# Kernel tuning notes

Hardware: AMD Instinct MI355X
Metric: run time of the kernel (lower is better)

## Reference

```python
import jax, jax.numpy as jnp
import numpy as np

B, R, A, S, SR = 128, 1024, 512, 196, 64


def _linear(x, w, b):
    return x @ w.T + b


def _lstm_cell(x, h, c, wih, whh, bih, bhh):
    # torch.nn.LSTMCell gate order: i, f, g, o
    g = x @ wih.T + bih + h @ whh.T + bhh
    i, f, gg, o = jnp.split(g, 4, axis=-1)
    c2 = jax.nn.sigmoid(f) * c + jax.nn.sigmoid(i) * jnp.tanh(gg)
    h2 = jax.nn.sigmoid(o) * jnp.tanh(c2)
    return h2, c2


def _attention(h, att_feats, p_att, mask, h2att_w, h2att_b, aw, ab):
    att_h = _linear(h, h2att_w, h2att_b)[:, None, :]            # [B,1,A]
    dot = jnp.tanh(p_att + att_h)                               # [B,S,A]
    e = jnp.einsum('bsa,a->bs', dot, aw[0]) + ab[0]             # alpha_net
    w = jax.nn.softmax(e, axis=1)
    w = w * mask
    w = w / jnp.sum(w, axis=1, keepdims=True)
    return jnp.einsum('bs,bsd->bd', w, att_feats)


def setup_inputs() -> dict:
    key = jax.random.key(0)
    ks = iter(jax.random.split(key, 80))
    def rn(shape, scale=1.0):
        return jax.random.normal(next(ks), shape, dtype=jnp.float32) * scale
    w = 0.02  # weight init scale
    inp = {
        'xt': rn((B, R)), 'state_h': rn((2, B, R)), 'state_c': rn((2, B, R)),
        'fc_feats': rn((B, R)),
        'att_feats': rn((B, S, R)), 'obj_feats': rn((B, S, R)),
        'attr_feats': rn((B, S, R)), 'rela_feats': rn((B, SR, R)),
        'p_obj_feats': rn((B, S, A)), 'p_attr_feats': rn((B, S, A)),
        'p_rela_feats': rn((B, SR, A)),
        'att_masks': jnp.ones((B, S), jnp.float32),
        'rela_masks': jnp.ones((B, SR), jnp.float32),
        'att_wih': rn((4*R, 3*R), w), 'att_whh': rn((4*R, R), w),
        'att_bih': rn((4*R,), w), 'att_bhh': rn((4*R,), w),
        'lang_wih': rn((4*R, 4*R), w), 'lang_whh': rn((4*R, R), w),
        'lang_bih': rn((4*R,), w), 'lang_bhh': rn((4*R,), w),
        'xt2_w': rn((R, R), w), 'xt2_b': rn((R,), w),
        'h_att2_w': rn((R, R), w), 'h_att2_b': rn((R,), w),
        'r_i2h_w': rn((R, 4*R), w), 'r_i2h_b': rn((R,), w),
        'r_h2h_w': rn((R, R), w), 'r_h2h_b': rn((R,), w),
        'huu_w': rn((R, 3*R), w), 'huu_b': rn((R,), w),
        'obj_h2att_w': rn((A, R), w), 'obj_h2att_b': rn((A,), w),
        'obj_alpha_w': rn((1, A), w), 'obj_alpha_b': rn((1,), w),
        'attr_h2att_w': rn((A, R), w), 'attr_h2att_b': rn((A,), w),
        'attr_alpha_w': rn((1, A), w), 'attr_alpha_b': rn((1,), w),
        'rela_h2att_w': rn((A, R), w), 'rela_h2att_b': rn((A,), w),
        'rela_alpha_w': rn((1, A), w), 'rela_alpha_b': rn((1,), w),
        'fr_lin_w': rn((R, R), w), 'fr_lin_b': rn((R,), w),
        'fr_emb_w': rn((R, R), w), 'fr_emb_b': rn((R,), w),
        'ho_lin_w': rn((R, R), w), 'ho_lin_b': rn((R,), w),
        'ho_emb_w': rn((R, R), w), 'ho_emb_b': rn((R,), w),
        'ada_alpha_w': rn((1, R), w), 'ada_alpha_b': rn((1,), w),
        'cfe_w': rn((R, A), w), 'cfe_b': rn((R,), w),
    }
    return inp


def reference(xt, state_h, state_c, fc_feats, att_feats, obj_feats, attr_feats,
              rela_feats, p_obj_feats, p_attr_feats, p_rela_feats, att_masks,
              rela_masks, att_wih, att_whh, att_bih, att_bhh, lang_wih,
              lang_whh, lang_bih, lang_bhh, xt2_w, xt2_b, h_att2_w, h_att2_b,
              r_i2h_w, r_i2h_b, r_h2h_w, r_h2h_b, huu_w, huu_b, obj_h2att_w,
              obj_h2att_b, obj_alpha_w, obj_alpha_b, attr_h2att_w,
              attr_h2att_b, attr_alpha_w, attr_alpha_b, rela_h2att_w,
              rela_h2att_b, rela_alpha_w, rela_alpha_b, fr_lin_w, fr_lin_b,
              fr_emb_w, fr_emb_b, ho_lin_w, ho_lin_b, ho_emb_w, ho_emb_b,
              ada_alpha_w, ada_alpha_b, cfe_w, cfe_b):
    # eval mode: all dropouts are identity
    prev_h = state_h[1]
    att_in = jnp.concatenate([prev_h, fc_feats, xt], axis=1)            # [B,3R]
    h_att_raw, c_att = _lstm_cell(att_in, state_h[0], state_c[0],
                                  att_wih, att_whh, att_bih, att_bhh)
    h_att = _linear(xt, xt2_w, xt2_b) + _linear(h_att_raw, h_att2_w, h_att2_b)
    att_obj = _attention(h_att, obj_feats, p_obj_feats, att_masks,
                         obj_h2att_w, obj_h2att_b, obj_alpha_w, obj_alpha_b)
    att_attr = _attention(h_att, attr_feats, p_attr_feats, att_masks,
                          attr_h2att_w, attr_h2att_b, attr_alpha_w, attr_alpha_b)
    att_rela = _attention(h_att, rela_feats, p_rela_feats, rela_masks,
                          rela_h2att_w, rela_h2att_b, rela_alpha_w, rela_alpha_b)
    lang_in = jnp.concatenate([h_att, att_obj, att_attr, att_rela], axis=1)  # [B,4R]
    h_lang, c_lang = _lstm_cell(lang_in, state_h[1], state_c[1],
                                lang_wih, lang_whh, lang_bih, lang_bhh)
    tanh_mt = jnp.tanh(c_lang)
    n5 = _linear(lang_in, r_i2h_w, r_i2h_b) + _linear(state_h[1], r_h2h_w, r_h2h_b)
    st = jax.nn.sigmoid(n5) * tanh_mt                                    # [B,R]
    # AdaAtt_attention(h_lang, st, att_feats, p_obj_feats)
    cfe = _linear(p_obj_feats, cfe_w, cfe_b)                             # [B,S,R]
    fake_region = jax.nn.relu(_linear(st, fr_lin_w, fr_lin_b))           # [B,R]
    fr_embed = _linear(fake_region, fr_emb_w, fr_emb_b)
    ho = jnp.tanh(_linear(h_lang, ho_lin_w, ho_lin_b))
    ho_embed = _linear(ho, ho_emb_w, ho_emb_b)
    img_all = jnp.concatenate([fake_region[:, None, :], att_feats], axis=1)    # [B,S+1,R]
    img_all_embed = jnp.concatenate([fr_embed[:, None, :], cfe], axis=1)
    hA = jnp.tanh(img_all_embed + ho_embed[:, None, :])
    e = jnp.einsum('bsr,r->bs', hA, ada_alpha_w[0]) + ada_alpha_b[0]
    PI = jax.nn.softmax(e, axis=1)                                       # [B,S+1]
    visAtt = jnp.einsum('bs,bsd->bd', PI, img_all)
    beta = PI[:, -1:]
    c_t_hat = beta * fake_region + (1.0 - beta) * visAtt
    output = _linear(jnp.concatenate([h_att, h_lang, c_t_hat], axis=1), huu_w, huu_b)
    new_h = jnp.stack([h_att, h_lang])
    new_c = jnp.stack([c_att, c_lang])
    return output, new_h, new_c
```

## Files before the change

kernel.cpp:

```cpp
#include <hip/hip_runtime.h>
#include <cstddef>

#define B 128
#define R 1024

typedef __attribute__((ext_vector_type(8))) short short8;
typedef __attribute__((ext_vector_type(4))) float f32x4;

__device__ __forceinline__ float sigf(float x) { return 1.0f / (1.0f + __expf(-x)); }

__device__ __forceinline__ short f2bf(float f) {
    unsigned int u = __float_as_uint(f);
    u += 0x7fff + ((u >> 16) & 1);
    return (short)(u >> 16);
}

__device__ __forceinline__ short8 cvt8(float4 u, float4 v) {
    short8 r;
    r[0] = f2bf(u.x); r[1] = f2bf(u.y); r[2] = f2bf(u.z); r[3] = f2bf(u.w);
    r[4] = f2bf(v.x); r[5] = f2bf(v.y); r[6] = f2bf(v.z); r[7] = f2bf(v.w);
    return r;
}

__device__ __forceinline__ void gll16(const void* g, void* l) {
    __builtin_amdgcn_global_load_lds(
        (const __attribute__((address_space(1))) unsigned int*)g,
        (__attribute__((address_space(3))) unsigned int*)l, 16, 0, 0);
}

struct GJob {
    const float* A1; const float* A2; const float* A3;
    const float* W1; const float* W2; const float* W3;
    float* C;
    int lda1, lda2, lda3;
    int ldw1, ldw2, ldw3;
    int K1, K12, Ktot;
    int ldc, Kchunk, nb;
};

__global__ __launch_bounds__(256) void gemm_sk_kernel(GJob j0, GJob j1, GJob j2, int njobs)
{
    GJob j = j0;
    int nbx = blockIdx.x;
    if (njobs > 1 && nbx >= j.nb) { nbx -= j.nb; j = j1; }
    if (njobs > 2 && nbx >= j.nb) { nbx -= j.nb; j = j2; }

    const int bn   = nbx * 64;
    const int kbeg = blockIdx.y * j.Kchunk;
    const int kend = kbeg + j.Kchunk;

    __shared__ short sA[128 * 40];
    __shared__ short sB[64 * 40];
    const int tid  = threadIdx.x;
    const int rA   = tid >> 1;
    const int kha  = (tid & 1) << 4;
    const int rB   = tid >> 2;
    const int khb  = (tid & 3) << 3;
    const int lane = tid & 63;
    const int wid  = tid >> 6;
    const int wm   = wid * 32;
    const int fr_  = lane & 15;
    const int kof  = (lane >> 4) * 8;

    f32x4 acc[2][4];
#pragma unroll
    for (int m = 0; m < 2; ++m)
#pragma unroll
        for (int n = 0; n < 4; ++n)
            acc[m][n] = (f32x4)0.0f;

    for (int k0 = kbeg; k0 < kend; k0 += 32) {
        int kgA = k0 + kha;
        const float* pa;
        if (kgA < j.K1)       pa = j.A1 + (size_t)rA * j.lda1 + kgA;
        else if (kgA < j.K12) pa = j.A2 + (size_t)rA * j.lda2 + (kgA - j.K1);
        else                  pa = j.A3 + (size_t)rA * j.lda3 + (kgA - j.K12);
        int kgB = k0 + khb;
        const float* pw;
        if (kgB < j.K1)       pw = j.W1 + (size_t)(bn + rB) * j.ldw1 + kgB;
        else if (kgB < j.K12) pw = j.W2 + (size_t)(bn + rB) * j.ldw2 + (kgB - j.K1);
        else                  pw = j.W3 + (size_t)(bn + rB) * j.ldw3 + (kgB - j.K12);

        float4 a0 = ((const float4*)pa)[0];
        float4 a1 = ((const float4*)pa)[1];
        float4 a2 = ((const float4*)pa)[2];
        float4 a3 = ((const float4*)pa)[3];
        float4 w0 = ((const float4*)pw)[0];
        float4 w1 = ((const float4*)pw)[1];
        __syncthreads();
        *(short8*)&sA[rA * 40 + kha]     = cvt8(a0, a1);
        *(short8*)&sA[rA * 40 + kha + 8] = cvt8(a2, a3);
        *(short8*)&sB[rB * 40 + khb]     = cvt8(w0, w1);
        __syncthreads();
        short8 af[2], bf[4];
#pragma unroll
        for (int m = 0; m < 2; ++m)
            af[m] = *(const short8*)&sA[(wm + m * 16 + fr_) * 40 + kof];
#pragma unroll
        for (int n = 0; n < 4; ++n)
            bf[n] = *(const short8*)&sB[(n * 16 + fr_) * 40 + kof];
#pragma unroll
        for (int m = 0; m < 2; ++m)
#pragma unroll
            for (int n = 0; n < 4; ++n)
                acc[m][n] = __builtin_amdgcn_mfma_f32_16x16x32_bf16(af[m], bf[n], acc[m][n], 0, 0, 0);
    }

#pragma unroll
    for (int m = 0; m < 2; ++m) {
        int row0 = wm + m * 16 + ((lane >> 4) << 2);
#pragma unroll
        for (int n = 0; n < 4; ++n) {
            int col = bn + n * 16 + fr_;
#pragma unroll
            for (int rg = 0; rg < 4; ++rg)
                atomicAdd(&j.C[(size_t)(row0 + rg) * j.ldc + col], acc[m][n][rg]);
        }
    }
}

__global__ __launch_bounds__(256) void tobf16_kernel(
    const float* __restrict__ P, const float* __restrict__ W,
    short* __restrict__ Pbf, short* __restrict__ Wbf)
{
    size_t base = ((size_t)blockIdx.x * 256 + threadIdx.x) * 8;
    if (base < 12845056) {
        float4 u = *(const float4*)(P + base);
        float4 v = *(const float4*)(P + base + 4);
        *(short8*)(Pbf + base) = cvt8(u, v);
    } else {
        size_t i = base - 12845056;
        float4 u = *(const float4*)(W + i);
        float4 v = *(const float4*)(W + i + 4);
        *(short8*)(Wbf + i) = cvt8(u, v);
    }
}

template <bool PRE>
__global__ __launch_bounds__(256) void cfe_v3_kernel(
    const float* __restrict__ P, const short* __restrict__ Pbf,
    const float* __restrict__ Wf, const short* __restrict__ Wbf,
    const float* __restrict__ cb, const float* __restrict__ hoe,
    const float* __restrict__ ho_b, const float* __restrict__ aw,
    float* __restrict__ e)
{
    int p = blockIdx.x;
    int x8 = p & 7, rest = p >> 3;
    int n8 = rest & 7, q = rest >> 3;
    int m = q * 8 + x8;
    if (m >= 196) return;
    const int bm = m * 128, bn = n8 * 128;

    __shared__ short sA[128 * 64];
    __shared__ short sB[128 * 64];
    const int tid  = threadIdx.x;
    const int lane = tid & 63;
    const int wid  = tid >> 6;
    const int wm   = (wid >> 1) * 64;
    const int wn   = (wid & 1) * 64;
    const int fr_  = lane & 15;
    const int kof  = (lane >> 4) * 8;

    f32x4 acc[4][4];
#pragma unroll
    for (int mi = 0; mi < 4; ++mi)
#pragma unroll
        for (int n = 0; n < 4; ++n)
            acc[mi][n] = (f32x4)0.0f;

    for (int k0 = 0; k0 < 512; k0 += 64) {
        __syncthreads();
        if (PRE) {
#pragma unroll
            for (int i = 0; i < 4; ++i) {
                const short* ga = Pbf + (size_t)(bm + i * 32 + (tid >> 3)) * 512 + k0 + (tid & 7) * 8;
                gll16(ga, sA + wid * 512 + i * 2048);
                const short* gw = Wbf + (size_t)(bn + i * 32 + (tid >> 3)) * 512 + k0 + (tid & 7) * 8;
                gll16(gw, sB + wid * 512 + i * 2048);
            }
        } else {
            int row = tid >> 1;
            int half = (tid & 1) * 32;
            const float* pa = P + (size_t)(bm + row) * 512 + k0 + half;
            const float* pw = Wf + (size_t)(bn + row) * 512 + k0 + half;
#pragma unroll
            for (int c = 0; c < 32; c += 8) {
                float4 u = *(const float4*)(pa + c);
                float4 v = *(const float4*)(pa + c + 4);
                *(short8*)&sA[row * 64 + half + c] = cvt8(u, v);
                float4 uw = *(const float4*)(pw + c);
                float4 vw = *(const float4*)(pw + c + 4);
                *(short8*)&sB[row * 64 + half + c] = cvt8(uw, vw);
            }
        }
        __syncthreads();
#pragma unroll
        for (int ks = 0; ks < 64; ks += 32) {
            short8 af[4], bf[4];
#pragma unroll
            for (int mi = 0; mi < 4; ++mi)
                af[mi] = *(const short8*)&sA[(wm + mi * 16 + fr_) * 64 + ks + kof];
#pragma unroll
            for (int n = 0; n < 4; ++n)
                bf[n] = *(const short8*)&sB[(wn + n * 16 + fr_) * 64 + ks + kof];
#pragma unroll
            for (int mi = 0; mi < 4; ++mi)
#pragma unroll
                for (int n = 0; n < 4; ++n)
                    acc[mi][n] = __builtin_amdgcn_mfma_f32_16x16x32_bf16(af[mi], bf[n], acc[mi][n], 0, 0, 0);
        }
    }

    const int l4 = lane >> 4;
    const int rbase = bm + wm + (l4 << 2);
    const int b0 = rbase / 196;
    const int b1 = (rbase + 51) / 196;
    float cba[4], awa[4], hv0[4], hv1[4];
#pragma unroll
    for (int n = 0; n < 4; ++n) {
        int col = bn + wn + n * 16 + fr_;
        cba[n] = cb[col] + ho_b[col];
        awa[n] = aw[col];
        hv0[n] = hoe[(size_t)b0 * R + col];
        hv1[n] = hoe[(size_t)b1 * R + col];
    }
#pragma unroll
    for (int mi = 0; mi < 4; ++mi) {
#pragma unroll
        for (int rg = 0; rg < 4; ++rg) {
            int gr = rbase + mi * 16 + rg;
            int b = gr / 196;
            bool second = (b != b0);
            float part = 0.0f;
#pragma unroll
            for (int n = 0; n < 4; ++n) {
                float hv = second ? hv1[n] : hv0[n];
                part += tanhf(acc[mi][n][rg] + cba[n] + hv) * awa[n];
            }
            part += __shfl_xor(part, 1);
            part += __shfl_xor(part, 2);
            part += __shfl_xor(part, 4);
            part += __shfl_xor(part, 8);
            if (fr_ == 0)
                atomicAdd(&e[b * 197 + 1 + (gr - b * 196)], part);
        }
    }
}

__global__ __launch_bounds__(256) void zero2_kernel(
    float* __restrict__ ws, int nws, float* __restrict__ o, const float* __restrict__ bias)
{
    int idx = blockIdx.x * 256 + threadIdx.x;
    if (idx < nws) ws[idx] = 0.0f;
    else { int i = idx - nws; o[i] = bias[i & 1023]; }
}

__global__ __launch_bounds__(256) void concat3_kernel(
    const float* __restrict__ a, const float* __restrict__ b2,
    const float* __restrict__ c, float* __restrict__ dst)
{
    int idx = blockIdx.x * 256 + threadIdx.x;
    int r = idx / 768, c4 = idx - r * 768;
    int col = c4 * 4;
    const float* src = (col < 1024) ? (a + (size_t)r * 1024 + col)
                     : (col < 2048) ? (b2 + (size_t)r * 1024 + col - 1024)
                                    : (c + (size_t)r * 1024 + col - 2048);
    *(float4*)(dst + (size_t)r * 3072 + col) = *(const float4*)src;
}

__global__ __launch_bounds__(256) void lstm_kernel(
    float* __restrict__ g, const float* __restrict__ bih, const float* __restrict__ bhh,
    const float* __restrict__ cprev, float* __restrict__ h, float* __restrict__ c,
    const float* __restrict__ n5, const float* __restrict__ nb1,
    const float* __restrict__ nb2, float* __restrict__ st)
{
    int idx = blockIdx.x * 256 + threadIdx.x;
    int b = idx >> 10, d = idx & 1023;
    float* gr = g + (size_t)b * 4096;
    float iv = sigf(gr[d]        + bih[d]        + bhh[d]);
    float fv = sigf(gr[1024 + d] + bih[1024 + d] + bhh[1024 + d]);
    float gv = tanhf(gr[2048 + d] + bih[2048 + d] + bhh[2048 + d]);
    float ov = sigf(gr[3072 + d] + bih[3072 + d] + bhh[3072 + d]);
    gr[d] = 0.0f; gr[1024 + d] = 0.0f; gr[2048 + d] = 0.0f; gr[3072 + d] = 0.0f;
    float c2 = fv * cprev[idx] + iv * gv;
    float tc = tanhf(c2);
    c[idx] = c2;
    h[idx] = ov * tc;
    if (st) st[idx] = sigf(n5[idx] + nb1[d] + nb2[d]) * tc;
}

__global__ __launch_bounds__(256) void hatt_epi_kernel(
    float* __restrict__ lang_in, const float* __restrict__ b1,
    const float* __restrict__ b2, float* __restrict__ h_att_out)
{
    int idx = blockIdx.x * 256 + threadIdx.x;
    int r = idx >> 10, c = idx & 1023;
    float v = lang_in[(size_t)r * 4096 + c] + b1[c] + b2[c];
    lang_in[(size_t)r * 4096 + c] = v;
    h_att_out[idx] = v;
}

__global__ __launch_bounds__(256) void att_e3_kernel(
    const float* __restrict__ p0, const float* __restrict__ p1, const float* __restrict__ p2,
    const float* __restrict__ ah3,
    const float* __restrict__ b0, const float* __restrict__ b1, const float* __restrict__ b2,
    const float* __restrict__ aw0, const float* __restrict__ aw1, const float* __restrict__ aw2,
    float* __restrict__ e3)
{
    int wid = threadIdx.x >> 6, lane = threadIdx.x & 63;
    int idx = blockIdx.x * 4 + wid;
    const float* p; const float* bb; const float* aw; int S, loc, mod;
    if (idx < 25088)      { mod = 0; loc = idx;          p = p0; bb = b0; aw = aw0; S = 196; }
    else if (idx < 50176) { mod = 1; loc = idx - 25088;  p = p1; bb = b1; aw = aw1; S = 196; }
    else                  { mod = 2; loc = idx - 50176;  p = p2; bb = b2; aw = aw2; S = 64; }
    int b = loc / S;
    const float4* pr = (const float4*)(p + (size_t)loc * 512);
    const float4* ab = (const float4*)(ah3 + (size_t)mod * 65536 + (size_t)b * 512);
    const float4* bb4 = (const float4*)bb;
    const float4* aw4 = (const float4*)aw;
    float sum = 0.0f;
#pragma unroll
    for (int k = 0; k < 2; ++k) {
        int a = k * 64 + lane;
        float4 pv = pr[a], av = ab[a], bv = bb4[a], wv = aw4[a];
        sum += tanhf(pv.x + av.x + bv.x) * wv.x;
        sum += tanhf(pv.y + av.y + bv.y) * wv.y;
        sum += tanhf(pv.z + av.z + bv.z) * wv.z;
        sum += tanhf(pv.w + av.w + bv.w) * wv.w;
    }
#pragma unroll
    for (int off = 32; off; off >>= 1) sum += __shfl_down(sum, off);
    if (lane == 0) e3[idx] = sum;
}

__global__ __launch_bounds__(256) void softmax3_kernel(
    float* __restrict__ e3, const float* __restrict__ am, const float* __restrict__ rm)
{
    __shared__ float red[256];
    int mod = blockIdx.x >> 7, b = blockIdx.x & 127, tid = threadIdx.x;
    int S = (mod == 2) ? 64 : 196;
    float* e = e3 + ((mod == 0) ? 0 : (mod == 1) ? 25088 : 50176) + (size_t)b * S;
    const float* mask = ((mod == 2) ? rm : am) + (size_t)b * S;
    float v = (tid < S) ? e[tid] : -3.4e38f;
    red[tid] = v; __syncthreads();
    for (int s = 128; s; s >>= 1) { if (tid < s) red[tid] = fmaxf(red[tid], red[tid + s]); __syncthreads(); }
    float m = red[0]; __syncthreads();
    float p = (tid < S) ? __expf(v - m) : 0.0f;
    red[tid] = p; __syncthreads();
    for (int s = 128; s; s >>= 1) { if (tid < s) red[tid] += red[tid + s]; __syncthreads(); }
    float s1 = red[0]; __syncthreads();
    float w = (tid < S) ? (p / s1) * mask[tid] : 0.0f;
    red[tid] = w; __syncthreads();
    for (int s = 128; s; s >>= 1) { if (tid < s) red[tid] += red[tid + s]; __syncthreads(); }
    float s2 = red[0];
    if (tid < S) e[tid] = w / s2;
}

__global__ __launch_bounds__(256) void wsum3_kernel(
    const float* __restrict__ e3,
    const float* __restrict__ f0, const float* __restrict__ f1, const float* __restrict__ f2,
    float* __restrict__ lang_in)
{
    int mod = blockIdx.x >> 7;
    int idx = (blockIdx.x & 127) * 256 + threadIdx.x;
    int b = idx >> 8, d4 = idx & 255;
    int S = (mod == 2) ? 64 : 196;
    int Sq = (S + 3) >> 2;
    int s0 = blockIdx.y * Sq, s1 = min(S, s0 + Sq);
    const float4* f = (const float4*)(((mod == 0) ? f0 : (mod == 1) ? f1 : f2) + ((size_t)b * S) * R) + d4;
    const float* wb = e3 + ((mod == 0) ? 0 : (mod == 1) ? 25088 : 50176) + (size_t)b * S;
    float4 acc = {0.f, 0.f, 0.f, 0.f};
#pragma unroll 4
    for (int s = s0; s < s1; ++s) {
        float w = wb[s];
        float4 fv = f[(size_t)s * 256];
        acc.x = fmaf(w, fv.x, acc.x); acc.y = fmaf(w, fv.y, acc.y);
        acc.z = fmaf(w, fv.z, acc.z); acc.w = fmaf(w, fv.w, acc.w);
    }
    float* dst = lang_in + (size_t)b * 4096 + 1024 + mod * 1024 + d4 * 4;
    atomicAdd(dst + 0, acc.x); atomicAdd(dst + 1, acc.y);
    atomicAdd(dst + 2, acc.z); atomicAdd(dst + 3, acc.w);
}

__global__ __launch_bounds__(256) void relutanh_kernel(
    float* __restrict__ fr, const float* __restrict__ frb,
    float* __restrict__ ho, const float* __restrict__ hob,
    float* __restrict__ ct_acc)
{
    int idx = blockIdx.x * 256 + threadIdx.x;
    int c = idx & 1023;
    if (idx < 131072) { fr[idx] = fmaxf(fr[idx] + frb[c], 0.0f); ct_acc[idx] = 0.0f; }
    else { int i = idx - 131072; ho[i] = tanhf(ho[i] + hob[c]); }
}

__global__ __launch_bounds__(256) void softmax_ada_kernel(
    float* __restrict__ e,
    const float* __restrict__ fre, const float* __restrict__ frb,
    const float* __restrict__ hoe, const float* __restrict__ hob,
    const float* __restrict__ aw)
{
    __shared__ float red[256];
    int b = blockIdx.x, tid = threadIdx.x;
    float s = 0.0f;
#pragma unroll
    for (int k = 0; k < 4; ++k) {
        int r = k * 256 + tid;
        s += tanhf(fre[(size_t)b * R + r] + frb[r] + hoe[(size_t)b * R + r] + hob[r]) * aw[r];
    }
    red[tid] = s; __syncthreads();
    for (int t = 128; t; t >>= 1) { if (tid < t) red[tid] += red[tid + t]; __syncthreads(); }
    float e0 = red[0]; __syncthreads();
    float v = (tid == 0) ? e0 : ((tid < 197) ? e[(size_t)b * 197 + tid] : -3.4e38f);
    red[tid] = v; __syncthreads();
    for (int t = 128; t; t >>= 1) { if (tid < t) red[tid] = fmaxf(red[tid], red[tid + t]); __syncthreads(); }
    float m = red[0]; __syncthreads();
    float p = (tid < 197) ? __expf(v - m) : 0.0f;
    red[tid] = p; __syncthreads();
    for (int t = 128; t; t >>= 1) { if (tid < t) red[tid] += red[tid + t]; __syncthreads(); }
    float s1 = red[0];
    if (tid < 197) e[(size_t)b * 197 + tid] = p / s1;
}

__global__ __launch_bounds__(256) void ct_part_kernel(
    const float* __restrict__ PI, const float* __restrict__ attf,
    float* __restrict__ ct_acc)
{
    int b = blockIdx.x, d4 = threadIdx.x;
    int s0 = blockIdx.y * 49, s1 = min(196, s0 + 49);
    const float* pb = PI + b * 197;
    const float4* af = (const float4*)(attf + ((size_t)b * 196) * R) + d4;
    float4 acc = {0.f, 0.f, 0.f, 0.f};
#pragma unroll 4
    for (int s = s0; s < s1; ++s) {
        float w = pb[1 + s];
        float4 av = af[(size_t)s * 256];
        acc.x = fmaf(w, av.x, acc.x); acc.y = fmaf(w, av.y, acc.y);
        acc.z = fmaf(w, av.z, acc.z); acc.w = fmaf(w, av.w, acc.w);
    }
    float* dst = ct_acc + (size_t)b * 1024 + d4 * 4;
    atomicAdd(dst + 0, acc.x); atomicAdd(dst + 1, acc.y);
    atomicAdd(dst + 2, acc.z); atomicAdd(dst + 3, acc.w);
}

__global__ __launch_bounds__(256) void ct_fin_kernel(
    const float* __restrict__ PI, const float* __restrict__ fr,
    const float* __restrict__ ct_acc, float* __restrict__ ct)
{
    int idx = blockIdx.x * 256 + threadIdx.x;
    int b = idx >> 10;
    const float* pb = PI + b * 197;
    float f = fr[idx];
    float acc = pb[0] * f + ct_acc[idx];
    float beta = pb[196];
    ct[idx] = beta * f + (1.0f - beta) * acc;
}

extern "C" void kernel_launch(void* const* d_in, const int* in_sizes, int n_in,
                              void* d_out, int out_size, void* d_ws, size_t ws_size,
                              hipStream_t stream)
{
    const float* xt         = (const float*)d_in[0];
    const float* state_h    = (const float*)d_in[1];
    const float* state_c    = (const float*)d_in[2];
    const float* fc_feats   = (const float*)d_in[3];
    const float* att_feats  = (const float*)d_in[4];
    const float* obj_feats  = (const float*)d_in[5];
    const float* attr_feats = (const float*)d_in[6];
    const float* rela_feats = (const float*)d_in[7];
    const float* p_obj      = (const float*)d_in[8];
    const float* p_attr     = (const float*)d_in[9];
    const float* p_rela     = (const float*)d_in[10];
    const float* att_masks  = (const float*)d_in[11];
    const float* rela_masks = (const float*)d_in[12];
    const float* att_wih    = (const float*)d_in[13];
    const float* att_whh    = (const float*)d_in[14];
    const float* att_bih    = (const float*)d_in[15];
    const float* att_bhh    = (const float*)d_in[16];
    const float* lang_wih   = (const float*)d_in[17];
    const float* lang_whh   = (const float*)d_in[18];
    const float* lang_bih   = (const float*)d_in[19];
    const float* lang_bhh   = (const float*)d_in[20];
    const float* xt2_w      = (const float*)d_in[21];
    const float* xt2_b      = (const float*)d_in[22];
    const float* h_att2_w   = (const float*)d_in[23];
    const float* h_att2_b   = (const float*)d_in[24];
    const float* r_i2h_w    = (const float*)d_in[25];
    const float* r_i2h_b    = (const float*)d_in[26];
    const float* r_h2h_w    = (const float*)d_in[27];
    const float* r_h2h_b    = (const float*)d_in[28];
    const float* huu_w      = (const float*)d_in[29];
    const float* huu_b      = (const float*)d_in[30];
    const float* obj_h2att_w  = (const float*)d_in[31];
    const float* obj_h2att_b  = (const float*)d_in[32];
    const float* obj_alpha_w  = (const float*)d_in[33];
    const float* attr_h2att_w = (const float*)d_in[35];
    const float* attr_h2att_b = (const float*)d_in[36];
    const float* attr_alpha_w = (const float*)d_in[37];
    const float* rela_h2att_w = (const float*)d_in[39];
    const float* rela_h2att_b = (const float*)d_in[40];
    const float* rela_alpha_w = (const float*)d_in[41];
    const float* fr_lin_w   = (const float*)d_in[43];
    const float* fr_lin_b   = (const float*)d_in[44];
    const float* fr_emb_w   = (const float*)d_in[45];
    const float* fr_emb_b   = (const float*)d_in[46];
    const float* ho_lin_w   = (const float*)d_in[47];
    const float* ho_lin_b   = (const float*)d_in[48];
    const float* ho_emb_w   = (const float*)d_in[49];
    const float* ho_emb_b   = (const float*)d_in[50];
    const float* ada_w      = (const float*)d_in[51];
    const float* cfe_w      = (const float*)d_in[53];
    const float* cfe_b      = (const float*)d_in[54];

    float* out = (float*)d_out;
    float* wsf = (float*)d_ws;

    float* g        = wsf + 0;
    float* lang_in  = wsf + 524288;
    float* att_h3   = wsf + 1048576;
    float* n5       = wsf + 1245184;
    float* fr       = wsf + 1376256;
    float* fre      = wsf + 1507328;
    float* ho       = wsf + 1638400;
    float* hoe      = wsf + 1769472;
    float* e_ada    = wsf + 1900544;
    const int NATOM = 1926144;
    float* att_in    = wsf + 1926144;
    float* ct_acc    = att_in;
    float* h_att_raw = wsf + 2319360;
    float* e3        = wsf + 2450432;
    float* st        = wsf + 2527232;
    float* ct        = wsf + 2658304;
    short* Pbf       = (short*)(wsf + 2789376);
    short* Wbf       = Pbf + 12845056;
    const bool big = ws_size >= (size_t)2789376 * 4 + (size_t)13369344 * 2;

    float* h_att_out  = out + 131072;
    float* h_lang_out = out + 262144;
    float* c_att_out  = out + 393216;
    float* c_lang_out = out + 524288;

    const float* prev_h = state_h + 131072;

    GJob Z = {};
    auto mk = [&](const float* A1, int lda1, int K1, const float* W1, int ldw1,
                  float* C, int ldc, int N, int Ktot, int Kchunk) {
        GJob j = Z;
        j.A1 = A1; j.lda1 = lda1; j.K1 = K1; j.K12 = Ktot; j.Ktot = Ktot;
        j.W1 = W1; j.ldw1 = ldw1;
        j.C = C; j.ldc = ldc; j.Kchunk = Kchunk; j.nb = N / 64;
        return j;
    };

    zero2_kernel<<<(NATOM + 131072) / 256, 256, 0, stream>>>(wsf, NATOM, out, huu_b);

    concat3_kernel<<<384, 256, 0, stream>>>(prev_h, fc_feats, xt, att_in);

    {
        GJob j = mk(att_in, 3072, 3072, att_wih, 3072, g, 4096, 4096, 4096, 1024);
        j.A2 = state_h; j.lda2 = 1024; j.W2 = att_whh; j.ldw2 = 1024; j.K12 = 4096;
        gemm_sk_kernel<<<dim3(64, 4), 256, 0, stream>>>(j, Z, Z, 1);
    }
    lstm_kernel<<<512, 256, 0, stream>>>(g, att_bih, att_bhh, state_c, h_att_raw, c_att_out,
                                         nullptr, nullptr, nullptr, nullptr);

    {
        GJob j = mk(xt, 1024, 1024, xt2_w, 1024, lang_in, 4096, 1024, 2048, 256);
        j.A2 = h_att_raw; j.lda2 = 1024; j.W2 = h_att2_w; j.ldw2 = 1024; j.K12 = 2048;
        gemm_sk_kernel<<<dim3(16, 8), 256, 0, stream>>>(j, Z, Z, 1);
    }
    hatt_epi_kernel<<<512, 256, 0, stream>>>(lang_in, xt2_b, h_att2_b, h_att_out);

    {
        GJob j0 = mk(lang_in, 4096, 1024, obj_h2att_w,  1024, att_h3 + 0,      512, 512, 1024, 128);
        GJob j1 = mk(lang_in, 4096, 1024, attr_h2att_w, 1024, att_h3 + 65536,  512, 512, 1024, 128);
        GJob j2 = mk(lang_in, 4096, 1024, rela_h2att_w, 1024, att_h3 + 131072, 512, 512, 1024, 128);
        gemm_sk_kernel<<<dim3(24, 8), 256, 0, stream>>>(j0, j1, j2, 3);
    }
    att_e3_kernel<<<14592, 256, 0, stream>>>(p_obj, p_attr, p_rela, att_h3,
        obj_h2att_b, attr_h2att_b, rela_h2att_b, obj_alpha_w, attr_alpha_w, rela_alpha_w, e3);
    softmax3_kernel<<<384, 256, 0, stream>>>(e3, att_masks, rela_masks);
    wsum3_kernel<<<dim3(384, 4), 256, 0, stream>>>(e3, obj_feats, attr_feats, rela_feats, lang_in);

    {
        GJob j0 = mk(lang_in, 4096, 4096, lang_wih, 4096, g, 4096, 4096, 5120, 1280);
        j0.A2 = prev_h; j0.lda2 = 1024; j0.W2 = lang_whh; j0.ldw2 = 1024; j0.K12 = 5120;
        GJob j1 = mk(lang_in, 4096, 4096, r_i2h_w, 4096, n5, 1024, 1024, 5120, 1280);
        j1.A2 = prev_h; j1.lda2 = 1024; j1.W2 = r_h2h_w; j1.ldw2 = 1024; j1.K12 = 5120;
        gemm_sk_kernel<<<dim3(80, 4), 256, 0, stream>>>(j0, j1, Z, 2);
    }
    lstm_kernel<<<512, 256, 0, stream>>>(g, lang_bih, lang_bhh, state_c + 131072,
                                         h_lang_out, c_lang_out, n5, r_i2h_b, r_h2h_b, st);

    {
        GJob j0 = mk(st, 1024, 1024, fr_lin_w, 1024, fr, 1024, 1024, 1024, 128);
        GJob j1 = mk(h_lang_out, 1024, 1024, ho_lin_w, 1024, ho, 1024, 1024, 1024, 128);
        gemm_sk_kernel<<<dim3(32, 8), 256, 0, stream>>>(j0, j1, Z, 2);
    }
    relutanh_kernel<<<1024, 256, 0, stream>>>(fr, fr_lin_b, ho, ho_lin_b, ct_acc);

    {
        GJob j0 = mk(fr, 1024, 1024, fr_emb_w, 1024, fre, 1024, 1024, 1024, 128);
        GJob j1 = mk(ho, 1024, 1024, ho_emb_w, 1024, hoe, 1024, 1024, 1024, 128);
        gemm_sk_kernel<<<dim3(32, 8), 256, 0, stream>>>(j0, j1, Z, 2);
    }
    if (big) {
        tobf16_kernel<<<6528, 256, 0, stream>>>(p_obj, cfe_w, Pbf, Wbf);
        cfe_v3_kernel<true><<<1600, 256, 0, stream>>>(p_obj, Pbf, cfe_w, Wbf,
            cfe_b, hoe, ho_emb_b, ada_w, e_ada);
    } else {
        cfe_v3_kernel<false><<<1600, 256, 0, stream>>>(p_obj, nullptr, cfe_w, nullptr,
            cfe_b, hoe, ho_emb_b, ada_w, e_ada);
    }
    softmax_ada_kernel<<<128, 256, 0, stream>>>(e_ada, fre, fr_emb_b, hoe, ho_emb_b, ada_w);
    ct_part_kernel<<<dim3(128, 4), 256, 0, stream>>>(e_ada, att_feats, ct_acc);
    ct_fin_kernel<<<512, 256, 0, stream>>>(e_ada, fr, ct_acc, ct);

    {
        GJob j = mk(lang_in, 4096, 1024, huu_w, 3072, out, 1024, 1024, 3072, 384);
        j.A2 = h_lang_out; j.lda2 = 1024; j.W2 = huu_w + 1024; j.ldw2 = 3072; j.K12 = 2048;
        j.A3 = ct; j.lda3 = 1024; j.W3 = huu_w + 2048; j.ldw3 = 3072;
        gemm_sk_kernel<<<dim3(16, 8), 256, 0, stream>>>(j, Z, Z, 1);
    }

    (void)in_sizes; (void)n_in; (void)out_size; (void)ws_size;
}
```

Before: 441.5 us.

## Merge prologue kernels, vectorise LSTM epilogues, reuse bf16 p_obj, double split-K

Zeroing, the input concat and the bf16 conversion are merged into one prologue launch. The LSTM and h_att epilogues are vectorised with float4. The obj attention score kernel now reads the bf16 copy of p_obj instead of the fp32 array, halving that traffic. Split-K factors for all GEMMs are doubled, and the ct_part grid is widened for more parallelism, at the cost of more atomics. The bf16 read lowers precision and depends on the bf16 buffer having been produced, which only happens when the big path is taken.

```diff
diff --git a/kernel.cpp b/kernel.cpp
--- a/kernel.cpp
+++ b/kernel.cpp
@@ -13,6 +13,11 @@
     unsigned int u = __float_as_uint(f);
     u += 0x7fff + ((u >> 16) & 1);
     return (short)(u >> 16);
+}
+
+__device__ __forceinline__ float bf2f(short s) {
+    unsigned int u = ((unsigned int)(unsigned short)s) << 16;
+    return __uint_as_float(u);
 }
 
 __device__ __forceinline__ short8 cvt8(float4 u, float4 v) {
@@ -119,11 +124,33 @@
     }
 }
 
-__global__ __launch_bounds__(256) void tobf16_kernel(
+__global__ __launch_bounds__(256) void prologue_kernel(
+    float* __restrict__ ws, int nws, float* __restrict__ o, const float* __restrict__ bias,
+    const float* __restrict__ ph, const float* __restrict__ fc, const float* __restrict__ xt,
+    float* __restrict__ att_in,
     const float* __restrict__ P, const float* __restrict__ W,
-    short* __restrict__ Pbf, short* __restrict__ Wbf)
-{
-    size_t base = ((size_t)blockIdx.x * 256 + threadIdx.x) * 8;
+    short* __restrict__ Pbf, short* __restrict__ Wbf, int ZB)
+{
+    int blk = blockIdx.x;
+    if (blk < ZB) {
+        int idx = blk * 256 + threadIdx.x;
+        if (idx < nws) ws[idx] = 0.0f;
+        else if (idx < nws + 131072) { int i = idx - nws; o[i] = bias[i & 1023]; }
+        return;
+    }
+    blk -= ZB;
+    if (blk < 384) {
+        int idx = blk * 256 + threadIdx.x;
+        int r = idx / 768, c4 = idx - r * 768;
+        int col = c4 * 4;
+        const float* src = (col < 1024) ? (ph + (size_t)r * 1024 + col)
+                         : (col < 2048) ? (fc + (size_t)r * 1024 + col - 1024)
+                                        : (xt + (size_t)r * 1024 + col - 2048);
+        *(float4*)(att_in + (size_t)r * 3072 + col) = *(const float4*)src;
+        return;
+    }
+    blk -= 384;
+    size_t base = ((size_t)blk * 256 + threadIdx.x) * 8;
     if (base < 12845056) {
         float4 u = *(const float4*)(P + base);
         float4 v = *(const float4*)(P + base + 4);
@@ -247,61 +274,74 @@
     }
 }
 
-__global__ __launch_bounds__(256) void zero2_kernel(
-    float* __restrict__ ws, int nws, float* __restrict__ o, const float* __restrict__ bias)
-{
-    int idx = blockIdx.x * 256 + threadIdx.x;
-    if (idx < nws) ws[idx] = 0.0f;
-    else { int i = idx - nws; o[i] = bias[i & 1023]; }
-}
-
-__global__ __launch_bounds__(256) void concat3_kernel(
-    const float* __restrict__ a, const float* __restrict__ b2,
-    const float* __restrict__ c, float* __restrict__ dst)
-{
-    int idx = blockIdx.x * 256 + threadIdx.x;
-    int r = idx / 768, c4 = idx - r * 768;
-    int col = c4 * 4;
-    const float* src = (col < 1024) ? (a + (size_t)r * 1024 + col)
-                     : (col < 2048) ? (b2 + (size_t)r * 1024 + col - 1024)
-                                    : (c + (size_t)r * 1024 + col - 2048);
-    *(float4*)(dst + (size_t)r * 3072 + col) = *(const float4*)src;
-}
-
 __global__ __launch_bounds__(256) void lstm_kernel(
     float* __restrict__ g, const float* __restrict__ bih, const float* __restrict__ bhh,
     const float* __restrict__ cprev, float* __restrict__ h, float* __restrict__ c,
     const float* __restrict__ n5, const float* __restrict__ nb1,
     const float* __restrict__ nb2, float* __restrict__ st)
 {
-    int idx = blockIdx.x * 256 + threadIdx.x;
-    int b = idx >> 10, d = idx & 1023;
+    int t = blockIdx.x * 256 + threadIdx.x;
+    int b = t >> 8, d4 = (t & 255) * 4;
     float* gr = g + (size_t)b * 4096;
-    float iv = sigf(gr[d]        + bih[d]        + bhh[d]);
-    float fv = sigf(gr[1024 + d] + bih[1024 + d] + bhh[1024 + d]);
-    float gv = tanhf(gr[2048 + d] + bih[2048 + d] + bhh[2048 + d]);
-    float ov = sigf(gr[3072 + d] + bih[3072 + d] + bhh[3072 + d]);
-    gr[d] = 0.0f; gr[1024 + d] = 0.0f; gr[2048 + d] = 0.0f; gr[3072 + d] = 0.0f;
-    float c2 = fv * cprev[idx] + iv * gv;
-    float tc = tanhf(c2);
-    c[idx] = c2;
-    h[idx] = ov * tc;
-    if (st) st[idx] = sigf(n5[idx] + nb1[d] + nb2[d]) * tc;
+    float4 gi = *(float4*)(gr + d4);
+    float4 gf = *(float4*)(gr + 1024 + d4);
+    float4 gg = *(float4*)(gr + 2048 + d4);
+    float4 go = *(float4*)(gr + 3072 + d4);
+    float4 bi1 = *(const float4*)(bih + d4),        bh1 = *(const float4*)(bhh + d4);
+    float4 bi2 = *(const float4*)(bih + 1024 + d4), bh2 = *(const float4*)(bhh + 1024 + d4);
+    float4 bi3 = *(const float4*)(bih + 2048 + d4), bh3 = *(const float4*)(bhh + 2048 + d4);
+    float4 bi4 = *(const float4*)(bih + 3072 + d4), bh4 = *(const float4*)(bhh + 3072 + d4);
+    float4 cp = *(const float4*)(cprev + (size_t)b * 1024 + d4);
+    float4 zero = {0.f, 0.f, 0.f, 0.f};
+    *(float4*)(gr + d4) = zero; *(float4*)(gr + 1024 + d4) = zero;
+    *(float4*)(gr + 2048 + d4) = zero; *(float4*)(gr + 3072 + d4) = zero;
+    float4 cc, hh;
+    float iv, fv, gv, ov, c2, tc;
+    iv = sigf(gi.x + bi1.x + bh1.x); fv = sigf(gf.x + bi2.x + bh2.x);
+    gv = tanhf(gg.x + bi3.x + bh3.x); ov = sigf(go.x + bi4.x + bh4.x);
+    c2 = fv * cp.x + iv * gv; tc = tanhf(c2); cc.x = c2; hh.x = ov * tc;
+    float tcx = tc;
+    iv = sigf(gi.y + bi1.y + bh1.y); fv = sigf(gf.y + bi2.y + bh2.y);
+    gv = tanhf(gg.y + bi3.y + bh3.y); ov = sigf(go.y + bi4.y + bh4.y);
+    c2 = fv * cp.y + iv * gv; tc = tanhf(c2); cc.y = c2; hh.y = ov * tc;
+    float tcy = tc;
+    iv = sigf(gi.z + bi1.z + bh1.z); fv = sigf(gf.z + bi2.z + bh2.z);
+    gv = tanhf(gg.z + bi3.z + bh3.z); ov = sigf(go.z + bi4.z + bh4.z);
+    c2 = fv * cp.z + iv * gv; tc = tanhf(c2); cc.z = c2; hh.z = ov * tc;
+    float tcz = tc;
+    iv = sigf(gi.w + bi1.w + bh1.w); fv = sigf(gf.w + bi2.w + bh2.w);
+    gv = tanhf(gg.w + bi3.w + bh3.w); ov = sigf(go.w + bi4.w + bh4.w);
+    c2 = fv * cp.w + iv * gv; tc = tanhf(c2); cc.w = c2; hh.w = ov * tc;
+    float tcw = tc;
+    *(float4*)(c + (size_t)b * 1024 + d4) = cc;
+    *(float4*)(h + (size_t)b * 1024 + d4) = hh;
+    if (st) {
+        float4 nv = *(const float4*)(n5 + (size_t)b * 1024 + d4);
+        float4 n1 = *(const float4*)(nb1 + d4), n2 = *(const float4*)(nb2 + d4);
+        float4 sv;
+        sv.x = sigf(nv.x + n1.x + n2.x) * tcx;
+        sv.y = sigf(nv.y + n1.y + n2.y) * tcy;
+        sv.z = sigf(nv.z + n1.z + n2.z) * tcz;
+        sv.w = sigf(nv.w + n1.w + n2.w) * tcw;
+        *(float4*)(st + (size_t)b * 1024 + d4) = sv;
+    }
 }
 
 __global__ __launch_bounds__(256) void hatt_epi_kernel(
     float* __restrict__ lang_in, const float* __restrict__ b1,
     const float* __restrict__ b2, float* __restrict__ h_att_out)
 {
-    int idx = blockIdx.x * 256 + threadIdx.x;
-    int r = idx >> 10, c = idx & 1023;
-    float v = lang_in[(size_t)r * 4096 + c] + b1[c] + b2[c];
-    lang_in[(size_t)r * 4096 + c] = v;
-    h_att_out[idx] = v;
+    int t = blockIdx.x * 256 + threadIdx.x;
+    int r = t >> 8, c4 = (t & 255) * 4;
+    float4 v = *(float4*)(lang_in + (size_t)r * 4096 + c4);
+    float4 x1 = *(const float4*)(b1 + c4), x2 = *(const float4*)(b2 + c4);
+    v.x += x1.x + x2.x; v.y += x1.y + x2.y; v.z += x1.z + x2.z; v.w += x1.w + x2.w;
+    *(float4*)(lang_in + (size_t)r * 4096 + c4) = v;
+    *(float4*)(h_att_out + (size_t)r * 1024 + c4) = v;
 }
 
 __global__ __launch_bounds__(256) void att_e3_kernel(
-    const float* __restrict__ p0, const float* __restrict__ p1, const float* __restrict__ p2,
+    const short* __restrict__ p0bf, const float* __restrict__ p1, const float* __restrict__ p2,
     const float* __restrict__ ah3,
     const float* __restrict__ b0, const float* __restrict__ b1, const float* __restrict__ b2,
     const float* __restrict__ aw0, const float* __restrict__ aw1, const float* __restrict__ aw2,
@@ -309,24 +349,39 @@
 {
     int wid = threadIdx.x >> 6, lane = threadIdx.x & 63;
     int idx = blockIdx.x * 4 + wid;
-    const float* p; const float* bb; const float* aw; int S, loc, mod;
-    if (idx < 25088)      { mod = 0; loc = idx;          p = p0; bb = b0; aw = aw0; S = 196; }
-    else if (idx < 50176) { mod = 1; loc = idx - 25088;  p = p1; bb = b1; aw = aw1; S = 196; }
-    else                  { mod = 2; loc = idx - 50176;  p = p2; bb = b2; aw = aw2; S = 64; }
-    int b = loc / S;
-    const float4* pr = (const float4*)(p + (size_t)loc * 512);
-    const float4* ab = (const float4*)(ah3 + (size_t)mod * 65536 + (size_t)b * 512);
-    const float4* bb4 = (const float4*)bb;
-    const float4* aw4 = (const float4*)aw;
     float sum = 0.0f;
-#pragma unroll
-    for (int k = 0; k < 2; ++k) {
-        int a = k * 64 + lane;
-        float4 pv = pr[a], av = ab[a], bv = bb4[a], wv = aw4[a];
-        sum += tanhf(pv.x + av.x + bv.x) * wv.x;
-        sum += tanhf(pv.y + av.y + bv.y) * wv.y;
-        sum += tanhf(pv.z + av.z + bv.z) * wv.z;
-        sum += tanhf(pv.w + av.w + bv.w) * wv.w;
+    if (idx < 25088) {
+        int b = idx / 196;
+        const short8 pv8 = *(const short8*)(p0bf + (size_t)idx * 512 + lane * 8);
+        const float4* ab = (const float4*)(ah3 + (size_t)b * 512) + lane * 2;
+        const float4* bb4 = (const float4*)b0 + lane * 2;
+        const float4* aw4 = (const float4*)aw0 + lane * 2;
+#pragma unroll
+        for (int k = 0; k < 2; ++k) {
+            float4 av = ab[k], bv = bb4[k], wv = aw4[k];
+            sum += tanhf(bf2f(pv8[k * 4 + 0]) + av.x + bv.x) * wv.x;
+            sum += tanhf(bf2f(pv8[k * 4 + 1]) + av.y + bv.y) * wv.y;
+            sum += tanhf(bf2f(pv8[k * 4 + 2]) + av.z + bv.z) * wv.z;
+            sum += tanhf(bf2f(pv8[k * 4 + 3]) + av.w + bv.w) * wv.w;
+        }
+    } else {
+        const float* p; const float* bb; const float* aw; int S, loc, mod;
+        if (idx < 50176) { mod = 1; loc = idx - 25088; p = p1; bb = b1; aw = aw1; S = 196; }
+        else             { mod = 2; loc = idx - 50176; p = p2; bb = b2; aw = aw2; S = 64; }
+        int b = loc / S;
+        const float4* pr = (const float4*)(p + (size_t)loc * 512);
+        const float4* ab = (const float4*)(ah3 + (size_t)mod * 65536 + (size_t)b * 512);
+        const float4* bb4 = (const float4*)bb;
+        const float4* aw4 = (const float4*)aw;
+#pragma unroll
+        for (int k = 0; k < 2; ++k) {
+            int a = k * 64 + lane;
+            float4 pv = pr[a], av = ab[a], bv = bb4[a], wv = aw4[a];
+            sum += tanhf(pv.x + av.x + bv.x) * wv.x;
+            sum += tanhf(pv.y + av.y + bv.y) * wv.y;
+            sum += tanhf(pv.z + av.z + bv.z) * wv.z;
+            sum += tanhf(pv.w + av.w + bv.w) * wv.w;
+        }
     }
 #pragma unroll
     for (int off = 32; off; off >>= 1) sum += __shfl_down(sum, off);
@@ -426,11 +481,11 @@
     float* __restrict__ ct_acc)
 {
     int b = blockIdx.x, d4 = threadIdx.x;
-    int s0 = blockIdx.y * 49, s1 = min(196, s0 + 49);
+    int s0 = blockIdx.y * 14, s1 = min(196, s0 + 14);
     const float* pb = PI + b * 197;
     const float4* af = (const float4*)(attf + ((size_t)b * 196) * R) + d4;
     float4 acc = {0.f, 0.f, 0.f, 0.f};
-#pragma unroll 4
+#pragma unroll 2
     for (int s = s0; s < s1; ++s) {
         float w = pb[1 + s];
         float4 av = af[(size_t)s * 256];
@@ -551,60 +606,62 @@
         return j;
     };
 
-    zero2_kernel<<<(NATOM + 131072) / 256, 256, 0, stream>>>(wsf, NATOM, out, huu_b);
-
-    concat3_kernel<<<384, 256, 0, stream>>>(prev_h, fc_feats, xt, att_in);
-
-    {
-        GJob j = mk(att_in, 3072, 3072, att_wih, 3072, g, 4096, 4096, 4096, 1024);
+    {
+        const int ZB = (NATOM + 131072) / 256;
+        int grid = ZB + 384 + (big ? 6528 : 0);
+        prologue_kernel<<<grid, 256, 0, stream>>>(wsf, NATOM, out, huu_b,
+            prev_h, fc_feats, xt, att_in, p_obj, cfe_w, Pbf, Wbf, ZB);
+    }
+
+    {
+        GJob j = mk(att_in, 3072, 3072, att_wih, 3072, g, 4096, 4096, 4096, 512);
         j.A2 = state_h; j.lda2 = 1024; j.W2 = att_whh; j.ldw2 = 1024; j.K12 = 4096;
-        gemm_sk_kernel<<<dim3(64, 4), 256, 0, stream>>>(j, Z, Z, 1);
-    }
-    lstm_kernel<<<512, 256, 0, stream>>>(g, att_bih, att_bhh, state_c, h_att_raw, c_att_out,
+        gemm_sk_kernel<<<dim3(64, 8), 256, 0, stream>>>(j, Z, Z, 1);
+    }
+    lstm_kernel<<<128, 256, 0, stream>>>(g, att_bih, att_bhh, state_c, h_att_raw, c_att_out,
                                          nullptr, nullptr, nullptr, nullptr);
 
     {
-        GJob j = mk(xt, 1024, 1024, xt2_w, 1024, lang_in, 4096, 1024, 2048, 256);
+        GJob j = mk(xt, 1024, 1024, xt2_w, 1024, lang_in, 4096, 1024, 2048, 128);
         j.A2 = h_att_raw; j.lda2 = 1024; j.W2 = h_att2_w; j.ldw2 = 1024; j.K12 = 2048;
-        gemm_sk_kernel<<<dim3(16, 8), 256, 0, stream>>>(j, Z, Z, 1);
-    }
-    hatt_epi_kernel<<<512, 256, 0, stream>>>(lang_in, xt2_b, h_att2_b, h_att_out);
-
-    {
-        GJob j0 = mk(lang_in, 4096, 1024, obj_h2att_w,  1024, att_h3 + 0,      512, 512, 1024, 128);
-        GJob j1 = mk(lang_in, 4096, 1024, attr_h2att_w, 1024, att_h3 + 65536,  512, 512, 1024, 128);
-        GJob j2 = mk(lang_in, 4096, 1024, rela_h2att_w, 1024, att_h3 + 131072, 512, 512, 1024, 128);
-        gemm_sk_kernel<<<dim3(24, 8), 256, 0, stream>>>(j0, j1, j2, 3);
-    }
-    att_e3_kernel<<<14592, 256, 0, stream>>>(p_obj, p_attr, p_rela, att_h3,
+        gemm_sk_kernel<<<dim3(16, 16), 256, 0, stream>>>(j, Z, Z, 1);
+    }
+    hatt_epi_kernel<<<128, 256, 0, stream>>>(lang_in, xt2_b, h_att2_b, h_att_out);
+
+    {
+        GJob j0 = mk(lang_in, 4096, 1024, obj_h2att_w,  1024, att_h3 + 0,      512, 512, 1024, 64);
+        GJob j1 = mk(lang_in, 4096, 1024, attr_h2att_w, 1024, att_h3 + 65536,  512, 512, 1024, 64);
+        GJob j2 = mk(lang_in, 4096, 1024, rela_h2att_w, 1024, att_h3 + 131072, 512, 512, 1024, 64);
+        gemm_sk_kernel<<<dim3(24, 16), 256, 0, stream>>>(j0, j1, j2, 3);
+    }
+    att_e3_kernel<<<14592, 256, 0, stream>>>(Pbf, p_attr, p_rela, att_h3,
         obj_h2att_b, attr_h2att_b, rela_h2att_b, obj_alpha_w, attr_alpha_w, rela_alpha_w, e3);
     softmax3_kernel<<<384, 256, 0, stream>>>(e3, att_masks, rela_masks);
     wsum3_kernel<<<dim3(384, 4), 256, 0, stream>>>(e3, obj_feats, attr_feats, rela_feats, lang_in);
 
     {
-        GJob j0 = mk(lang_in, 4096, 4096, lang_wih, 4096, g, 4096, 4096, 5120, 1280);
+        GJob j0 = mk(lang_in, 4096, 4096, lang_wih, 4096, g, 4096, 4096, 5120, 640);
         j0.A2 = prev_h; j0.lda2 = 1024; j0.W2 = lang_whh; j0.ldw2 = 1024; j0.K12 = 5120;
-        GJob j1 = mk(lang_in, 4096, 4096, r_i2h_w, 4096, n5, 1024, 1024, 5120, 1280);
+        GJob j1 = mk(lang_in, 4096, 4096, r_i2h_w, 4096, n5, 1024, 1024, 5120, 640);
         j1.A2 = prev_h; j1.lda2 = 1024; j1.W2 = r_h2h_w; j1.ldw2 = 1024; j1.K12 = 5120;
-        gemm_sk_kernel<<<dim3(80, 4), 256, 0, stream>>>(j0, j1, Z, 2);
-    }
-    lstm_kernel<<<512, 256, 0, stream>>>(g, lang_bih, lang_bhh, state_c + 131072,
+        gemm_sk_kernel<<<dim3(80, 8), 256, 0, stream>>>(j0, j1, Z, 2);
+    }
+    lstm_kernel<<<128, 256, 0, stream>>>(g, lang_bih, lang_bhh, state_c + 131072,
                                          h_lang_out, c_lang_out, n5, r_i2h_b, r_h2h_b, st);
 
     {
-        GJob j0 = mk(st, 1024, 1024, fr_lin_w, 1024, fr, 1024, 1024, 1024, 128);
-        GJob j1 = mk(h_lang_out, 1024, 1024, ho_lin_w, 1024, ho, 1024, 1024, 1024, 128);
-        gemm_sk_kernel<<<dim3(32, 8), 256, 0, stream>>>(j0, j1, Z, 2);
+        GJob j0 = mk(st, 1024, 1024, fr_lin_w, 1024, fr, 1024, 1024, 1024, 64);
+        GJob j1 = mk(h_lang_out, 1024, 1024, ho_lin_w, 1024, ho, 1024, 1024, 1024, 64);
+        gemm_sk_kernel<<<dim3(32, 16), 256, 0, stream>>>(j0, j1, Z, 2);
     }
     relutanh_kernel<<<1024, 256, 0, stream>>>(fr, fr_lin_b, ho, ho_lin_b, ct_acc);
 
     {
-        GJob j0 = mk(fr, 1024, 1024, fr_emb_w, 1024, fre, 1024, 1024, 1024, 128);
-        GJob j1 = mk(ho, 1024, 1024, ho_emb_w, 1024, hoe, 1024, 1024, 1024, 128);
-        gemm_sk_kernel<<<dim3(32, 8), 256, 0, stream>>>(j0, j1, Z, 2);
+        GJob j0 = mk(fr, 1024, 1024, fr_emb_w, 1024, fre, 1024, 1024, 1024, 64);
+        GJob j1 = mk(ho, 1024, 1024, ho_emb_w, 1024, hoe, 1024, 1024, 1024, 64);
+        gemm_sk_kernel<<<dim3(32, 16), 256, 0, stream>>>(j0, j1, Z, 2);
     }
     if (big) {
-        tobf16_kernel<<<6528, 256, 0, stream>>>(p_obj, cfe_w, Pbf, Wbf);
         cfe_v3_kernel<true><<<1600, 256, 0, stream>>>(p_obj, Pbf, cfe_w, Wbf,
             cfe_b, hoe, ho_emb_b, ada_w, e_ada);
     } else {
@@ -612,14 +669,14 @@
             cfe_b, hoe, ho_emb_b, ada_w, e_ada);
     }
     softmax_ada_kernel<<<128, 256, 0, stream>>>(e_ada, fre, fr_emb_b, hoe, ho_emb_b, ada_w);
-    ct_part_kernel<<<dim3(128, 4), 256, 0, stream>>>(e_ada, att_feats, ct_acc);
+    ct_part_kernel<<<dim3(128, 14), 256, 0, stream>>>(e_ada, att_feats, ct_acc);
     ct_fin_kernel<<<512, 256, 0, stream>>>(e_ada, fr, ct_acc, ct);
 
     {
-        GJob j = mk(lang_in, 4096, 1024, huu_w, 3072, out, 1024, 1024, 3072, 384);
+        GJob j = mk(lang_in, 4096, 1024, huu_w, 3072, out, 1024, 1024, 3072, 192);
         j.A2 = h_lang_out; j.lda2 = 1024; j.W2 = huu_w + 1024; j.ldw2 = 3072; j.K12 = 2048;
         j.A3 = ct; j.lda3 = 1024; j.W3 = huu_w + 2048; j.ldw3 = 3072;
-        gemm_sk_kernel<<<dim3(16, 8), 256, 0, stream>>>(j, Z, Z, 1);
+        gemm_sk_kernel<<<dim3(16, 16), 256, 0, stream>>>(j, Z, Z, 1);
     }
 
     (void)in_sizes; (void)n_in; (void)out_size; (void)ws_size;
```

Measured after the change: 430.2 us. 2.6% less time.
